# Kernel tuning notes

Hardware: AMD Instinct MI355X
Metric: run time of the kernel (lower is better)

Reference implementation:

```python
import jax, jax.numpy as jnp
import numpy as np

EPS = 1e-9
TEMP = 1.0
TOP_K = 2


def setup_inputs() -> dict:
    key = jax.random.key(0)
    k1, k2, k3, k4 = jax.random.split(key, 4)
    B, T, D, DC, E = 8, 4096, 1024, 512, 64
    din = D + DC
    inputs = jax.random.normal(k1, (B, T, D), dtype=jnp.float32)
    cond = jax.random.normal(k2, (B, T, DC), dtype=jnp.float32)
    # CondRouterMLP params (bias=False): Linear(din -> 2*din), GELU, Linear(2*din -> E)
    W1 = jax.random.normal(k3, (2 * din, din), dtype=jnp.float32) / np.sqrt(din).astype(np.float32)
    W2 = jax.random.normal(k4, (E, 2 * din), dtype=jnp.float32) / np.sqrt(2 * din).astype(np.float32)
    return {"inputs": inputs, "cond": cond, "W1": W1, "W2": W2}


def reference(inputs, cond, W1, W2):
    B, T, D = inputs.shape
    # concat hidden states with condition, flatten tokens
    x = jnp.concatenate([inputs, cond], axis=-1).reshape(-1, D + cond.shape[-1])  # [N, din]
    h = jax.nn.gelu(x @ W1.T, approximate=False)          # [N, 2*din] (torch nn.GELU = exact erf)
    logits = h @ W2.T                                     # [N, E]
    logits = (logits - logits.max(axis=-1, keepdims=True)) / TEMP
    probs = jax.nn.softmax(logits, axis=-1) + EPS
    probs = jnp.clip(probs, EPS, 1.0 - EPS)               # [N, E]
    # eval-mode top-k selection
    top_v, top_i = jax.lax.top_k(probs, TOP_K)            # [N, k]
    N, E = probs.shape
    rows = jnp.arange(N)[:, None]
    router_mask = jnp.zeros_like(probs).at[rows, top_i].set(1.0)
    router_probs = jnp.zeros_like(probs).at[rows, top_i].set(top_v)
    router_probs = router_probs / router_probs.sum(axis=-1, keepdims=True)  # normalize=True
    return (
        router_mask.reshape(B, T, E),
        top_i.reshape(B, T, TOP_K),
        router_probs.reshape(B, T, E),
        probs.reshape(B, T, E),
    )
```

## Files before the change

kernel.cpp:

```cpp
#include <hip/hip_runtime.h>
#include <cmath>

#define N_TOK 32768
#define D0    1024
#define DCC   512
#define DIN   1536
#define JD    3072
#define NE    64
#define BM    128
#define BJ    256
#define BK    32
#define NJC   (JD/BJ)
#define NIT   (DIN/BK)
#define NTH   512
#define HS    36
#define EPSV  1e-9f

typedef _Float16 half8 __attribute__((ext_vector_type(8)));
typedef float    f32x4 __attribute__((ext_vector_type(4)));

#define SZ_A  16384
#define SZ_B  32768
#define OFF_A 0
#define OFF_B 32768
#define LDS_TOTAL 131072
#define OFF_H    32768
#define OFF_LRED 0
#define OFF_EPI  36864

#define W1T_G (192*3072)
#define W2T_G (384*64)

__device__ __forceinline__ f32x4 mfma16(half8 a, half8 b, f32x4 c) {
    return __builtin_amdgcn_mfma_f32_16x16x32_f16(a, b, c, 0, 0, 0);
}

__device__ __forceinline__ void split8(const float4 v0, const float4 v1, half8& hh, half8& hl) {
    float f[8] = {v0.x, v0.y, v0.z, v0.w, v1.x, v1.y, v1.z, v1.w};
    #pragma unroll
    for (int i = 0; i < 8; ++i) {
        _Float16 h = (_Float16)f[i];
        hh[i] = h;
        hl[i] = (_Float16)(f[i] - (float)h);
    }
}

__device__ __forceinline__ void gload16(const void* g, void* l) {
    __builtin_amdgcn_global_load_lds(
        (const __attribute__((address_space(1))) unsigned int*)g,
        (__attribute__((address_space(3))) unsigned int*)l, 16, 0, 0);
}

#define SOFT_BARRIER() do { \
    asm volatile("s_waitcnt lgkmcnt(0)" ::: "memory"); \
    __builtin_amdgcn_s_barrier(); \
} while (0)

__global__ void presplit_w1t(const float* __restrict__ W1,
                             _Float16* __restrict__ hi, _Float16* __restrict__ lo) {
    int g = blockIdx.x * blockDim.x + threadIdx.x;
    if (g >= W1T_G) return;
    const int j  = g % JD;
    const int ko = g / JD;
    const float* src = W1 + (size_t)j * DIN + ko * 8;
    float4 v0 = *(const float4*)src;
    float4 v1 = *(const float4*)(src + 4);
    half8 h, l;
    split8(v0, v1, h, l);
    *(half8*)(hi + (size_t)g * 8) = h;
    *(half8*)(lo + (size_t)g * 8) = l;
}

__global__ void presplit_w2t(const float* __restrict__ W2,
                             _Float16* __restrict__ hi, _Float16* __restrict__ lo) {
    int g = blockIdx.x * blockDim.x + threadIdx.x;
    if (g >= W2T_G) return;
    const int e  = g & 63;
    const int jo = g >> 6;
    const float* src = W2 + (size_t)e * JD + jo * 8;
    float4 v0 = *(const float4*)src;
    float4 v1 = *(const float4*)(src + 4);
    half8 h, l;
    split8(v0, v1, h, l);
    *(half8*)(hi + (size_t)g * 8) = h;
    *(half8*)(lo + (size_t)g * 8) = l;
}

__global__ __launch_bounds__(NTH, 1)
void router_v11(const float* __restrict__ inp, const float* __restrict__ cnd,
                const _Float16* __restrict__ W1h, const _Float16* __restrict__ W1l,
                const _Float16* __restrict__ W2h, const _Float16* __restrict__ W2l,
                float* __restrict__ out_mask, float* __restrict__ out_topi,
                float* __restrict__ out_rp, float* __restrict__ out_probs)
{
    __shared__ __align__(16) char smem[LDS_TOTAL];

    const int tid  = threadIdx.x;
    const int lane = tid & 63;
    const int w    = tid >> 6;
    const int tg   = w >> 2;
    const int jg   = w & 3;
    const int l15  = lane & 15;
    const int lg   = lane >> 4;
    const int t0   = blockIdx.x * BM;

    const int akoct = w >> 1;
    const int arow  = (w & 1) * 64 + lane;
    const int bplane = w >> 2;
    const int bkoct  = w & 3;

    int aoff[4], boff[4];
    #pragma unroll
    for (int tf = 0; tf < 4; ++tf) aoff[tf] = (lg*128 + tg*64 + tf*16 + l15) * 16;
    #pragma unroll
    for (int jf = 0; jf < 4; ++jf) boff[jf] = (lg*256 + jg*64 + jf*16 + l15) * 16;

    const f32x4 vzero = {0.f, 0.f, 0.f, 0.f};
    f32x4 lacc[4] = {vzero, vzero, vzero, vzero};

    const float* const xrowA = inp + (size_t)(t0 + arow) * D0;
    const float* const xrowC = cnd + (size_t)(t0 + arow) * DCC;
    const _Float16* const Wbp = bplane ? W1l : W1h;

    _Float16* const myHh = (_Float16*)(smem + OFF_H + w * 9216);
    _Float16* const myHl = myHh + 2304;

    for (int jc = 0; jc < NJC; ++jc) {
        f32x4 acc1[4][4];
        #pragma unroll
        for (int tf = 0; tf < 4; ++tf)
            #pragma unroll
            for (int jf = 0; jf < 4; ++jf) acc1[tf][jf] = vzero;

        {
            float4 v0 = *(const float4*)(xrowA + akoct * 8);
            float4 v1 = *(const float4*)(xrowA + akoct * 8 + 4);
            #pragma unroll
            for (int d = 0; d < 2; ++d) {
                const int ko = d * 4 + bkoct;
                const _Float16* src = Wbp + ((size_t)ko * JD + jc * BJ) * 8;
                char* dst = smem + OFF_B + d * SZ_B + (bplane * 4 + bkoct) * 4096;
                #pragma unroll
                for (int q = 0; q < 4; ++q)
                    gload16(src + (size_t)(q * 64 + lane) * 8, dst + q * 1024);
            }
            half8 hh, hl;
            split8(v0, v1, hh, hl);
            const int g = (akoct * 128 + arow) * 16;
            *(half8*)(smem + OFF_A + g) = hh;
            *(half8*)(smem + OFF_A + 8192 + g) = hl;
            asm volatile("s_waitcnt vmcnt(0) lgkmcnt(0)" ::: "memory");
            __builtin_amdgcn_s_barrier();
        }

        for (int it = 0; it < NIT; ++it) {
            const bool haveA = (it + 1 < NIT);
            const bool haveB = (it + 2 < NIT);
            float4 xv0, xv1;
            if (haveA) {
                const int k = (it + 1) * BK + akoct * 8;
                const float* sx = (k < D0) ? (xrowA + k) : (xrowC + k - D0);
                xv0 = *(const float4*)sx;
                xv1 = *(const float4*)(sx + 4);
                __builtin_amdgcn_sched_barrier(0);
            }
            if (haveB) {
                const int ko = (it + 2) * 4 + bkoct;
                const _Float16* src = Wbp + ((size_t)ko * JD + jc * BJ) * 8;
                char* dst = smem + OFF_B + ((it + 2) % 3) * SZ_B
                          + (bplane * 4 + bkoct) * 4096;
                #pragma unroll
                for (int q = 0; q < 4; ++q)
                    gload16(src + (size_t)(q * 64 + lane) * 8, dst + q * 1024);
            }
            const char* ab = smem + OFF_A + (it & 1) * SZ_A;
            const char* bb = smem + OFF_B + (it % 3) * SZ_B;
            half8 ah[4], al[4], bh[4], bl[4];
            #pragma unroll
            for (int tf = 0; tf < 4; ++tf) {
                ah[tf] = *(const half8*)(ab + aoff[tf]);
                al[tf] = *(const half8*)(ab + 8192 + aoff[tf]);
            }
            #pragma unroll
            for (int jf = 0; jf < 4; ++jf) {
                bh[jf] = *(const half8*)(bb + boff[jf]);
                bl[jf] = *(const half8*)(bb + 16384 + boff[jf]);
            }
            #pragma unroll
            for (int tf = 0; tf < 4; ++tf)
                #pragma unroll
                for (int jf = 0; jf < 4; ++jf) {
                    acc1[tf][jf] = mfma16(ah[tf], bh[jf], acc1[tf][jf]);
                    acc1[tf][jf] = mfma16(ah[tf], bl[jf], acc1[tf][jf]);
                    acc1[tf][jf] = mfma16(al[tf], bh[jf], acc1[tf][jf]);
                }
            if (haveA) {
                half8 hh, hl;
                split8(xv0, xv1, hh, hl);
                char* nab = smem + OFF_A + ((it + 1) & 1) * SZ_A;
                const int g = (akoct * 128 + arow) * 16;
                *(half8*)(nab + g) = hh;
                *(half8*)(nab + 8192 + g) = hl;
            }
            if (it < NIT - 1) {
                SOFT_BARRIER();
            } else {
                __syncthreads();
            }
        }

        #pragma unroll
        for (int r = 0; r < 2; ++r) {
            #pragma unroll
            for (int c = 0; c < 2; ++c) {
                const int jf = 2*r + c;
                #pragma unroll
                for (int tf = 0; tf < 4; ++tf)
                    #pragma unroll
                    for (int rr = 0; rr < 4; ++rr) {
                        const float v = acc1[tf][jf][rr];
                        const float gv = 0.5f * v * (1.0f + erff(v * 0.70710678118654752f));
                        const _Float16 gh = (_Float16)gv;
                        const _Float16 gl = (_Float16)(gv - (float)gh);
                        const int o = (tf*16 + lg*4 + rr) * HS + c*16 + l15;
                        myHh[o] = gh; myHl[o] = gl;
                    }
            }
            __syncthreads();
            #pragma unroll
            for (int s = 0; s < 4; ++s) {
                const _Float16* sh = (const _Float16*)(smem + OFF_H + (tg*4 + s) * 9216);
                const _Float16* sl = sh + 2304;
                const int jo = jc*32 + s*8 + r*4 + lg;
                const size_t wg = ((size_t)jo * 64 + jg*16 + l15) * 8;
                half8 b2h = *(const half8*)(W2h + wg);
                half8 b2l = *(const half8*)(W2l + wg);
                #pragma unroll
                for (int tf = 0; tf < 4; ++tf) {
                    const int o = (tf*16 + l15) * HS + lg*8;
                    half8 a2h = *(const half8*)(sh + o);
                    half8 a2l = *(const half8*)(sl + o);
                    lacc[tf] = mfma16(a2h, b2h, lacc[tf]);
                    lacc[tf] = mfma16(a2h, b2l, lacc[tf]);
                    lacc[tf] = mfma16(a2l, b2h, lacc[tf]);
                }
            }
            __syncthreads();
        }
    }

    float* const Lred = (float*)(smem + OFF_LRED);
    #pragma unroll
    for (int tf = 0; tf < 4; ++tf)
        #pragma unroll
        for (int rr = 0; rr < 4; ++rr)
            Lred[(tg*64 + tf*16 + lg*4 + rr) * 68 + jg*16 + l15] = lacc[tf][rr];
    __syncthreads();

    float* const mA   = (float*)(smem + OFF_EPI);
    float* const invA = mA + BM;
    int*   const i1A  = (int*)(invA + BM);
    int*   const i2A  = i1A + BM;
    float* const rp1A = (float*)(i2A + BM);
    float* const rp2A = rp1A + BM;

    if (tid < BM) {
        const float* row = Lred + tid * 68;
        float m = -3.402823466e38f;
        for (int e = 0; e < NE; ++e) m = fmaxf(m, row[e]);
        float s = 0.f, v1 = -3.402823466e38f, v2 = -3.402823466e38f;
        int i1 = 0, i2 = 0;
        for (int e = 0; e < NE; ++e) {
            const float v = row[e];
            s += expf(v - m);
            if (v > v1)      { v2 = v1; i2 = i1; v1 = v; i1 = e; }
            else if (v > v2) { v2 = v; i2 = e; }
        }
        const float inv = 1.f / s;
        const float p1 = fminf(expf(v1 - m) * inv + EPSV, 1.f - EPSV);
        const float p2 = fminf(expf(v2 - m) * inv + EPSV, 1.f - EPSV);
        mA[tid] = m; invA[tid] = inv; i1A[tid] = i1; i2A[tid] = i2;
        const float den = p1 + p2;
        rp1A[tid] = p1 / den; rp2A[tid] = p2 / den;
    }
    __syncthreads();

    for (int idx = tid; idx < BM * NE; idx += NTH) {
        const int r = idx >> 6, e = idx & 63;
        const size_t o = (size_t)(t0 + r) * NE + e;
        const float p = fminf(expf(Lred[r * 68 + e] - mA[r]) * invA[r] + EPSV, 1.f - EPSV);
        const int b1 = (e == i1A[r]), b2 = (e == i2A[r]);
        out_probs[o] = p;
        out_mask[o]  = (b1 | b2) ? 1.f : 0.f;
        out_rp[o]    = b1 ? rp1A[r] : (b2 ? rp2A[r] : 0.f);
    }
    if (tid < BM * 2) {
        const int r = tid >> 1, q = tid & 1;
        out_topi[(size_t)(t0 + r) * 2 + q] = (float)(q ? i2A[r] : i1A[r]);
    }
}

extern "C" void kernel_launch(void* const* d_in, const int* in_sizes, int n_in,
                              void* d_out, int out_size, void* d_ws, size_t ws_size,
                              hipStream_t stream) {
    const float* inp = (const float*)d_in[0];
    const float* cnd = (const float*)d_in[1];
    const float* W1  = (const float*)d_in[2];
    const float* W2  = (const float*)d_in[3];

    float* out = (float*)d_out;
    const size_t NT = (size_t)N_TOK;
    float* out_mask  = out;
    float* out_topi  = out + NT * NE;
    float* out_rp    = out + NT * NE + NT * 2;
    float* out_probs = out + NT * NE + NT * 2 + NT * NE;

    _Float16* W1h = (_Float16*)d_ws;
    _Float16* W1l = W1h + (size_t)W1T_G * 8;
    _Float16* W2h = W1l + (size_t)W1T_G * 8;
    _Float16* W2l = W2h + (size_t)W2T_G * 8;

    hipLaunchKernelGGL(presplit_w1t, dim3((W1T_G + 255) / 256), dim3(256), 0, stream, W1, W1h, W1l);
    hipLaunchKernelGGL(presplit_w2t, dim3((W2T_G + 255) / 256), dim3(256), 0, stream, W2, W2h, W2l);
    hipLaunchKernelGGL(router_v11, dim3(N_TOK / BM), dim3(NTH), 0, stream,
                       inp, cnd, W1h, W1l, W2h, W2l,
                       out_mask, out_topi, out_rp, out_probs);
}
```

Before: 1.228 ms.

## Split GEMM main loop into four barrier-fenced phases interleaving loads with MFMA

Restructures the inner K loop into four sub-phases, one per token fragment. Each phase loads one A fragment, issues part of the next B tile's global-to-LDS copies or the A split/store, then runs its MFMA group under raised wave priority (s_setprio) between workgroup barriers. This is meant to overlap LDS and global traffic with matrix math across waves and to cut register pressure by holding one A fragment at a time. The cost is many more barriers per iteration, and the vmcnt handling has changed, which risks hazards or stalls.

```diff
diff --git a/kernel.cpp b/kernel.cpp
--- a/kernel.cpp
+++ b/kernel.cpp
@@ -31,6 +31,10 @@
 #define W1T_G (192*3072)
 #define W2T_G (384*64)
 
+#define SBAR()   __builtin_amdgcn_s_barrier()
+#define LGKM0()  asm volatile("s_waitcnt lgkmcnt(0)" ::: "memory")
+#define SCHEDB() __builtin_amdgcn_sched_barrier(0)
+
 __device__ __forceinline__ f32x4 mfma16(half8 a, half8 b, f32x4 c) {
     return __builtin_amdgcn_mfma_f32_16x16x32_f16(a, b, c, 0, 0, 0);
 }
@@ -50,11 +54,6 @@
         (const __attribute__((address_space(1))) unsigned int*)g,
         (__attribute__((address_space(3))) unsigned int*)l, 16, 0, 0);
 }
-
-#define SOFT_BARRIER() do { \
-    asm volatile("s_waitcnt lgkmcnt(0)" ::: "memory"); \
-    __builtin_amdgcn_s_barrier(); \
-} while (0)
 
 __global__ void presplit_w1t(const float* __restrict__ W1,
                              _Float16* __restrict__ hi, _Float16* __restrict__ lo) {
@@ -87,7 +86,7 @@
 }
 
 __global__ __launch_bounds__(NTH, 1)
-void router_v11(const float* __restrict__ inp, const float* __restrict__ cnd,
+void router_v13(const float* __restrict__ inp, const float* __restrict__ cnd,
                 const _Float16* __restrict__ W1h, const _Float16* __restrict__ W1l,
                 const _Float16* __restrict__ W2h, const _Float16* __restrict__ W2l,
                 float* __restrict__ out_mask, float* __restrict__ out_topi,
@@ -125,6 +124,8 @@
     _Float16* const myHh = (_Float16*)(smem + OFF_H + w * 9216);
     _Float16* const myHl = myHh + 2304;
 
+    const int agbyte = (akoct * 128 + arow) * 16;
+
     for (int jc = 0; jc < NJC; ++jc) {
         f32x4 acc1[4][4];
         #pragma unroll
@@ -146,68 +147,108 @@
             }
             half8 hh, hl;
             split8(v0, v1, hh, hl);
-            const int g = (akoct * 128 + arow) * 16;
-            *(half8*)(smem + OFF_A + g) = hh;
-            *(half8*)(smem + OFF_A + 8192 + g) = hl;
-            asm volatile("s_waitcnt vmcnt(0) lgkmcnt(0)" ::: "memory");
-            __builtin_amdgcn_s_barrier();
+            *(half8*)(smem + OFF_A + agbyte) = hh;
+            *(half8*)(smem + OFF_A + 8192 + agbyte) = hl;
+            asm volatile("s_waitcnt vmcnt(4)" ::: "memory");
+            LGKM0();
+            SBAR();
         }
 
         for (int it = 0; it < NIT; ++it) {
             const bool haveA = (it + 1 < NIT);
             const bool haveB = (it + 2 < NIT);
+            const char* ab = smem + OFF_A + (it & 1) * SZ_A;
+            const char* bb = smem + OFF_B + (it % 3) * SZ_B;
+            char* nab = smem + OFF_A + ((it + 1) & 1) * SZ_A;
+            char* bdst = smem + OFF_B + ((it + 2) % 3) * SZ_B
+                       + (bplane * 4 + bkoct) * 4096;
+            const _Float16* bsrc = Wbp +
+                ((size_t)((it + 2) * 4 + bkoct) * JD + jc * BJ) * 8;
+
+            half8 bh[4], bl[4], ah, al;
             float4 xv0, xv1;
+
+            #pragma unroll
+            for (int jf = 0; jf < 4; ++jf) {
+                bh[jf] = *(const half8*)(bb + boff[jf]);
+                bl[jf] = *(const half8*)(bb + 16384 + boff[jf]);
+            }
+            ah = *(const half8*)(ab + aoff[0]);
+            al = *(const half8*)(ab + 8192 + aoff[0]);
             if (haveA) {
                 const int k = (it + 1) * BK + akoct * 8;
                 const float* sx = (k < D0) ? (xrowA + k) : (xrowC + k - D0);
                 xv0 = *(const float4*)sx;
                 xv1 = *(const float4*)(sx + 4);
-                __builtin_amdgcn_sched_barrier(0);
-            }
+            }
+            SCHEDB();
             if (haveB) {
-                const int ko = (it + 2) * 4 + bkoct;
-                const _Float16* src = Wbp + ((size_t)ko * JD + jc * BJ) * 8;
-                char* dst = smem + OFF_B + ((it + 2) % 3) * SZ_B
-                          + (bplane * 4 + bkoct) * 4096;
-                #pragma unroll
-                for (int q = 0; q < 4; ++q)
-                    gload16(src + (size_t)(q * 64 + lane) * 8, dst + q * 1024);
-            }
-            const char* ab = smem + OFF_A + (it & 1) * SZ_A;
-            const char* bb = smem + OFF_B + (it % 3) * SZ_B;
-            half8 ah[4], al[4], bh[4], bl[4];
-            #pragma unroll
-            for (int tf = 0; tf < 4; ++tf) {
-                ah[tf] = *(const half8*)(ab + aoff[tf]);
-                al[tf] = *(const half8*)(ab + 8192 + aoff[tf]);
-            }
-            #pragma unroll
-            for (int jf = 0; jf < 4; ++jf) {
-                bh[jf] = *(const half8*)(bb + boff[jf]);
-                bl[jf] = *(const half8*)(bb + 16384 + boff[jf]);
-            }
-            #pragma unroll
-            for (int tf = 0; tf < 4; ++tf)
-                #pragma unroll
-                for (int jf = 0; jf < 4; ++jf) {
-                    acc1[tf][jf] = mfma16(ah[tf], bh[jf], acc1[tf][jf]);
-                    acc1[tf][jf] = mfma16(ah[tf], bl[jf], acc1[tf][jf]);
-                    acc1[tf][jf] = mfma16(al[tf], bh[jf], acc1[tf][jf]);
-                }
+                gload16(bsrc + (size_t)lane * 8, bdst);
+                gload16(bsrc + (size_t)(64 + lane) * 8, bdst + 1024);
+            }
+            SBAR(); LGKM0(); SCHEDB();
+            __builtin_amdgcn_s_setprio(1);
+            #pragma unroll
+            for (int jf = 0; jf < 4; ++jf) {
+                acc1[0][jf] = mfma16(ah, bh[jf], acc1[0][jf]);
+                acc1[0][jf] = mfma16(ah, bl[jf], acc1[0][jf]);
+                acc1[0][jf] = mfma16(al, bh[jf], acc1[0][jf]);
+            }
+            __builtin_amdgcn_s_setprio(0);
+            SBAR();
+
+            ah = *(const half8*)(ab + aoff[1]);
+            al = *(const half8*)(ab + 8192 + aoff[1]);
+            if (haveB) {
+                gload16(bsrc + (size_t)(128 + lane) * 8, bdst + 2048);
+                gload16(bsrc + (size_t)(192 + lane) * 8, bdst + 3072);
+            }
+            SBAR(); LGKM0(); SCHEDB();
+            __builtin_amdgcn_s_setprio(1);
+            #pragma unroll
+            for (int jf = 0; jf < 4; ++jf) {
+                acc1[1][jf] = mfma16(ah, bh[jf], acc1[1][jf]);
+                acc1[1][jf] = mfma16(ah, bl[jf], acc1[1][jf]);
+                acc1[1][jf] = mfma16(al, bh[jf], acc1[1][jf]);
+            }
+            __builtin_amdgcn_s_setprio(0);
+            SBAR();
+
+            ah = *(const half8*)(ab + aoff[2]);
+            al = *(const half8*)(ab + 8192 + aoff[2]);
             if (haveA) {
                 half8 hh, hl;
                 split8(xv0, xv1, hh, hl);
-                char* nab = smem + OFF_A + ((it + 1) & 1) * SZ_A;
-                const int g = (akoct * 128 + arow) * 16;
-                *(half8*)(nab + g) = hh;
-                *(half8*)(nab + 8192 + g) = hl;
-            }
-            if (it < NIT - 1) {
-                SOFT_BARRIER();
-            } else {
-                __syncthreads();
-            }
+                *(half8*)(nab + agbyte) = hh;
+                *(half8*)(nab + 8192 + agbyte) = hl;
+            }
+            SBAR(); LGKM0(); SCHEDB();
+            __builtin_amdgcn_s_setprio(1);
+            #pragma unroll
+            for (int jf = 0; jf < 4; ++jf) {
+                acc1[2][jf] = mfma16(ah, bh[jf], acc1[2][jf]);
+                acc1[2][jf] = mfma16(ah, bl[jf], acc1[2][jf]);
+                acc1[2][jf] = mfma16(al, bh[jf], acc1[2][jf]);
+            }
+            __builtin_amdgcn_s_setprio(0);
+            SBAR();
+
+            ah = *(const half8*)(ab + aoff[3]);
+            al = *(const half8*)(ab + 8192 + aoff[3]);
+            SBAR(); LGKM0(); SCHEDB();
+            __builtin_amdgcn_s_setprio(1);
+            #pragma unroll
+            for (int jf = 0; jf < 4; ++jf) {
+                acc1[3][jf] = mfma16(ah, bh[jf], acc1[3][jf]);
+                acc1[3][jf] = mfma16(ah, bl[jf], acc1[3][jf]);
+                acc1[3][jf] = mfma16(al, bh[jf], acc1[3][jf]);
+            }
+            __builtin_amdgcn_s_setprio(0);
+            SBAR();
         }
+
+        asm volatile("s_waitcnt vmcnt(0)" ::: "memory");
+        __syncthreads();
 
         #pragma unroll
         for (int r = 0; r < 2; ++r) {
@@ -322,7 +363,7 @@
 
     hipLaunchKernelGGL(presplit_w1t, dim3((W1T_G + 255) / 256), dim3(256), 0, stream, W1, W1h, W1l);
     hipLaunchKernelGGL(presplit_w2t, dim3((W2T_G + 255) / 256), dim3(256), 0, stream, W2, W2h, W2l);
-    hipLaunchKernelGGL(router_v11, dim3(N_TOK / BM), dim3(NTH), 0, stream,
+    hipLaunchKernelGGL(router_v13, dim3(N_TOK / BM), dim3(NTH), 0, stream,
                        inp, cnd, W1h, W1l, W2h, W2l,
                        out_mask, out_topi, out_rp, out_probs);
 }
```

New measurement: 1.237 ms. About the same (+0.7%).
